# Kernel tuning notes

Hardware: AMD Instinct MI355X
Metric: run time of the kernel (lower is better)

The kernel has to match this reference:

```python
import jax, jax.numpy as jnp
import numpy as np

N = 20000        # nodes
E = 320000       # edges (avg degree 16)
D_IN = 64        # CFG.feature_dim
D_H = 128        # CFG.hidden_dim
T = 20           # CFG.ode_time_points
MIN_DEPTH, MAX_DEPTH = 0.1, 3.0
EPS = 1e-5       # torch LayerNorm default


def setup_inputs() -> dict:
    key = jax.random.key(0)
    ks = jax.random.split(key, 10)
    def rn(k, shape, fan_in):
        return jax.random.normal(k, shape, jnp.float32) / np.float32(np.sqrt(fan_in))
    return {
        "x": jax.random.normal(ks[0], (N, D_IN), jnp.float32),
        "edge_index": jax.random.randint(ks[1], (2, E), 0, N, dtype=jnp.int32),
        # input projection: Linear(64,128) + LayerNorm(128)
        "Wi": rn(ks[2], (D_IN, D_H), D_IN), "bi": jnp.zeros((D_H,), jnp.float32),
        "ln_in_g": jnp.ones((D_H,), jnp.float32), "ln_in_b": jnp.zeros((D_H,), jnp.float32),
        # epigenetic params (init zeros as in module)
        "meth": jnp.zeros((D_H,), jnp.float32), "hist": jnp.zeros((4,), jnp.float32),
        # 3 GCNConv(128,128) + LayerNorm(128)
        "gcn_w": rn(ks[3], (3, D_H, D_H), D_H), "gcn_b": jnp.zeros((3, D_H), jnp.float32),
        "ln_g": jnp.ones((3, D_H), jnp.float32), "ln_b": jnp.zeros((3, D_H), jnp.float32),
        # gate: Linear(256,128) + Sigmoid
        "gate_w": rn(ks[4], (2 * D_H, D_H), 2 * D_H), "gate_b": jnp.zeros((D_H,), jnp.float32),
        "res_w": jnp.float32(0.1),
        "log_depth": jnp.float32(0.0),
        # output projection: Linear(128,128) + LayerNorm(128)
        "Wo": rn(ks[5], (D_H, D_H), D_H), "bo": jnp.zeros((D_H,), jnp.float32),
        "ln_out_g": jnp.ones((D_H,), jnp.float32), "ln_out_b": jnp.zeros((D_H,), jnp.float32),
    }


def layernorm(x, g, b):
    mu = x.mean(-1, keepdims=True)
    var = ((x - mu) ** 2).mean(-1, keepdims=True)
    return (x - mu) * jax.lax.rsqrt(var + EPS) * g + b


def _forward(x, edge_index, Wi, bi, ln_in_g, ln_in_b, meth, hist,
             gcn_w, gcn_b, ln_g, ln_b, gate_w, gate_b, res_w, log_depth,
             Wo, bo, ln_out_g, ln_out_b):
    row, col = edge_index[0], edge_index[1]  # source -> target
    # GCN symmetric normalization (no self loops): 1/sqrt(deg_i deg_j)
    deg = jax.ops.segment_sum(jnp.ones((E,), jnp.float32), col, num_segments=N)
    dis = jnp.where(deg > 0, jax.lax.rsqrt(jnp.maximum(deg, 1.0)), 0.0)
    norm = (dis[row] * dis[col])[:, None]  # [E,1]

    def gcn(h, W, b):
        m = (h @ W)[row] * norm                      # [E, D_H] gather
        return jax.ops.segment_sum(m, col, num_segments=N) + b  # scatter

    # input projection (dropout is identity in eval)
    h = jax.nn.relu(layernorm(x @ Wi + bi, ln_in_g, ln_in_b))

    # epigenetic regulation (chromatin accessibility uses .item() in torch -> stop_gradient)
    meth_sil = jax.nn.sigmoid(meth).mean()
    hs = jax.nn.sigmoid(hist)
    act = (hs[0] + hs[2]) / 2
    rep = (hs[1] + hs[3]) / 2
    access = jax.lax.stop_gradient(jnp.clip(act - rep + 0.5, 0.0, 1.0))
    h = h * (access * (1.0 - meth_sil))

    # ODE dynamics dh/dt
    def f(hh):
        h0 = hh
        hc = hh
        for i in range(3):
            hn = layernorm(gcn(hc, gcn_w[i], gcn_b[i]), ln_g[i], ln_b[i])
            if i > 0:
                gate = jax.nn.sigmoid(jnp.concatenate([hc, hn], -1) @ gate_w + gate_b)
                hc = gate * hn + (1.0 - gate) * hc
            else:
                hc = hn
        hc = jnp.tanh(hc)
        return hc + res_w * h0

    depth = jnp.clip(jnp.exp(log_depth), MIN_DEPTH, MAX_DEPTH)
    dt = depth / (T - 1)

    def step(hh, _):
        k1 = f(hh)
        k2 = f(hh + 0.5 * dt * k1)
        k3 = f(hh + 0.5 * dt * k2)
        k4 = f(hh + dt * k3)
        return hh + (dt / 6.0) * (k1 + 2.0 * k2 + 2.0 * k3 + k4), None

    h_final, _ = jax.lax.scan(step, h, None, length=T - 1)

    h_out = layernorm(h_final @ Wo + bo, ln_out_g, ln_out_b)
    return h_out.mean(axis=0, keepdims=True)  # batch=None -> global mean pool [1, D_H]


def reference(x, edge_index, Wi, bi, ln_in_g, ln_in_b, meth, hist,
              gcn_w, gcn_b, ln_g, ln_b, gate_w, gate_b, res_w, log_depth,
              Wo, bo, ln_out_g, ln_out_b):
    return _forward(x, edge_index, Wi, bi, ln_in_g, ln_in_b, meth, hist,
                    gcn_w, gcn_b, ln_g, ln_b, gate_w, gate_b, res_w, log_depth,
                    Wo, bo, ln_out_g, ln_out_b)
```

## Files before the change

### kernel.cpp

```cpp
#include <hip/hip_runtime.h>

typedef unsigned int u32;
using bf16x8 = __attribute__((ext_vector_type(8))) short;
using f32x4  = __attribute__((ext_vector_type(4))) float;
using f32x2  = __attribute__((ext_vector_type(2))) float;

#define NN 20000
#define EE 320000
#define DH 128
#define DIN 64
#define TSTEPS 20
#define LNEPS 1e-5f
#define NCHUNK 1250

__device__ __forceinline__ u32 f2bf(float f) {
    u32 x = __float_as_uint(f);
    return (x + 0x7fffu + ((x >> 16) & 1u)) >> 16;
}
__device__ __forceinline__ float bflo(u32 p) { return __uint_as_float(p << 16); }
__device__ __forceinline__ float bfhi(u32 p) { return __uint_as_float(p & 0xffff0000u); }
__device__ __forceinline__ u32 packbf(float a, float b) { return f2bf(a) | (f2bf(b) << 16); }
__device__ __forceinline__ float wredsum(float v) {
#pragma unroll
    for (int m = 32; m >= 1; m >>= 1) v += __shfl_xor(v, m, 64);
    return v;
}
__device__ __forceinline__ float sigm(float x) { return 1.f / (1.f + __expf(-x)); }

__device__ __forceinline__ void accum8_fp8(float* a, uint2 q, float w) {
    f32x2 c01 = __builtin_amdgcn_cvt_pk_f32_fp8((int)q.x, false);
    f32x2 c23 = __builtin_amdgcn_cvt_pk_f32_fp8((int)q.x, true);
    f32x2 c45 = __builtin_amdgcn_cvt_pk_f32_fp8((int)q.y, false);
    f32x2 c67 = __builtin_amdgcn_cvt_pk_f32_fp8((int)q.y, true);
    a[0] += w * c01[0]; a[1] += w * c01[1];
    a[2] += w * c23[0]; a[3] += w * c23[1];
    a[4] += w * c45[0]; a[5] += w * c45[1];
    a[6] += w * c67[0]; a[7] += w * c67[1];
}

__device__ __forceinline__ void store_dual(u32* dstb, u32* dst8, int node, int j, int sub, float o) {
    float po = __shfl_xor(o, 1, 64);
    if (!(sub & 1)) dstb[node * 64 + j * 8 + (sub >> 1)] = packbf(o, po);
    int pk = __builtin_amdgcn_cvt_pk_fp8_f32(o, po, 0, false);
    int pk2 = __shfl_xor(pk, 2, 64);
    if (!(sub & 3)) dst8[node * 32 + j * 4 + (sub >> 2)] = (u32)(pk & 0xffff) | ((u32)pk2 << 16);
}

__global__ void k_init(int* deg, float* oacc) {
    int i = blockIdx.x * blockDim.x + threadIdx.x;
    if (i < NN) deg[i] = 0;
    if (i < DH) oacc[i] = 0.f;
}

__global__ void k_scalars(const float* meth, const float* hist, const float* logd,
                          const float* resw, float* sc) {
    float msum = 0.f;
    for (int j = 0; j < DH; j++) msum += sigm(meth[j]);
    float msil = msum * (1.f / DH);
    float h0 = sigm(hist[0]), h1 = sigm(hist[1]), h2 = sigm(hist[2]), h3 = sigm(hist[3]);
    float act = 0.5f * (h0 + h2), rep = 0.5f * (h1 + h3);
    float access = fminf(fmaxf(act - rep + 0.5f, 0.f), 1.f);
    sc[0] = access * (1.f - msil);
    float depth = fminf(fmaxf(__expf(logd[0]), 0.1f), 3.f);
    sc[1] = depth / (float)(TSTEPS - 1);
    sc[2] = resw[0];
}

__global__ void k_deg(const int* col, int* deg) {
    int e = blockIdx.x * blockDim.x + threadIdx.x;
    if (e < EE) atomicAdd(&deg[col[e]], 1);
}

__global__ __launch_bounds__(1024) void k_scan(const int* deg, int* offs, int* cursor, float* dis) {
    __shared__ int part[1024];
    const int CH = (NN + 1023) / 1024;
    int t = threadIdx.x;
    int base = t * CH;
    int s = 0;
    for (int k = 0; k < CH; k++) { int i = base + k; if (i < NN) s += deg[i]; }
    part[t] = s;
    __syncthreads();
    for (int off = 1; off < 1024; off <<= 1) {
        int v = part[t];
        int add = (t >= off) ? part[t - off] : 0;
        __syncthreads();
        part[t] = v + add;
        __syncthreads();
    }
    int run = part[t] - s;
    for (int k = 0; k < CH; k++) {
        int i = base + k;
        if (i < NN) {
            offs[i] = run; cursor[i] = run;
            int d = deg[i];
            run += d;
            dis[i] = (d > 0) ? rsqrtf((float)d) : 0.f;
        }
    }
    if (t == 1023) offs[NN] = run;
}

__global__ void k_scatter(const int* row, const int* col, int* cursor, const float* dis,
                          u32* epk) {
    int e = blockIdx.x * blockDim.x + threadIdx.x;
    if (e < EE) {
        int c = col[e], r = row[e];
        int pos = atomicAdd(&cursor[c], 1);
        epk[pos] = (f2bf(dis[r] * dis[c]) << 16) | (u32)r;
    }
}

__global__ void k_pack(const float* gcnw, const float* gatew, const float* Wo,
                       u32* wfrag, u32* gfrag, u32* wopk) {
    int tid = blockIdx.x * blockDim.x + threadIdx.x;
    if (tid < 6144) {
        int lane = tid & 63, rem = tid >> 6;
        int j = rem & 7; rem >>= 3;
        int q = rem & 3; int l = rem >> 2;
        const float* W = gcnw + l * DH * DH;
        int r0 = 32 * q + 8 * (lane >> 4);
        int c  = 16 * j + (lane & 15);
        u32* o = wfrag + tid * 4;
#pragma unroll
        for (int p = 0; p < 4; p++)
            o[p] = packbf(W[(r0 + 2 * p) * DH + c], W[(r0 + 2 * p + 1) * DH + c]);
    } else if (tid < 6144 + 4096) {
        int t = tid - 6144;
        int lane = t & 63, rem = t >> 6;
        int j = rem & 7, q = rem >> 3;
        int r0 = 32 * q + 8 * (lane >> 4);
        int c  = 16 * j + (lane & 15);
        u32* o = gfrag + t * 4;
#pragma unroll
        for (int p = 0; p < 4; p++)
            o[p] = packbf(gatew[(r0 + 2 * p) * DH + c], gatew[(r0 + 2 * p + 1) * DH + c]);
    } else if (tid < 6144 + 4096 + 8192) {
        int t = tid - 10240;
        int k2 = t / DH, j = t % DH;
        wopk[t] = packbf(Wo[(2 * k2) * DH + j], Wo[(2 * k2 + 1) * DH + j]);
    }
}

__global__ __launch_bounds__(1024) void k_inproj(const float* x, const float* Wi, const float* bi,
                                                 const float* g, const float* b, const float* sc,
                                                 u32* y, u32* y8, float* hh) {
    __shared__ float Wl[DIN * DH];
    for (int i = threadIdx.x; i < DIN * DH; i += 1024) Wl[i] = Wi[i];
    __syncthreads();
    int wv = threadIdx.x >> 6, t = threadIdx.x & 63;
    int n = blockIdx.x * 16 + wv;
    if (n >= NN) return;
    float xv = x[n * DIN + t];
    float2 bb = *(const float2*)&bi[2 * t];
    float y0 = bb.x, y1 = bb.y;
#pragma unroll
    for (int k = 0; k < DIN; k++) {
        float a = __shfl(xv, k, 64);
        float2 w = *(const float2*)&Wl[k * DH + 2 * t];
        y0 += a * w.x; y1 += a * w.y;
    }
    float mu = wredsum(y0 + y1) * (1.f / DH);
    float d0 = y0 - mu, d1 = y1 - mu;
    float var = wredsum(d0 * d0 + d1 * d1) * (1.f / DH);
    float r = rsqrtf(var + LNEPS);
    float2 gg = *(const float2*)&g[2 * t], lb = *(const float2*)&b[2 * t];
    float scale = sc[0];
    float v0 = fmaxf(d0 * r * gg.x + lb.x, 0.f) * scale;
    float v1 = fmaxf(d1 * r * gg.y + lb.y, 0.f) * scale;
    y[n * 64 + t] = packbf(v0, v1);
    *(float2*)&hh[n * DH + 2 * t] = make_float2(v0, v1);
    int pk = __builtin_amdgcn_cvt_pk_fp8_f32(v0, v1, 0, false);
    int pk2 = __shfl_xor(pk, 1, 64);
    if (!(t & 1)) y8[n * 32 + (t >> 1)] = (u32)(pk & 0xffff) | ((u32)pk2 << 16);
}

__device__ __forceinline__ void gather_row(const u32* __restrict__ src8, u32* tile,
                                           int row, int sub, int qb, int e0, int e1,
                                           const u32* __restrict__ epk) {
    float a[8] = {0.f, 0.f, 0.f, 0.f, 0.f, 0.f, 0.f, 0.f};
    for (int eb = e0; eb < e1; eb += 16) {
        int cc = min(16, e1 - eb);
        u32 p = 0;
        if (sub < cc) p = epk[eb + sub];
        {
            u32 pe[8]; uint2 q[8];
#pragma unroll
            for (int u = 0; u < 8; u++) pe[u] = (u32)__shfl((int)p, qb + u, 64);
#pragma unroll
            for (int u = 0; u < 8; u++)
                q[u] = *(const uint2*)(src8 + (pe[u] & 0xffffu) * 32 + sub * 2);
#pragma unroll
            for (int u = 0; u < 8; u++)
                accum8_fp8(a, q[u], __uint_as_float(pe[u] & 0xffff0000u));
        }
        if (cc > 8) {
            u32 pe[8]; uint2 q[8];
#pragma unroll
            for (int u = 0; u < 8; u++) pe[u] = (u32)__shfl((int)p, qb + 8 + u, 64);
#pragma unroll
            for (int u = 0; u < 8; u++)
                q[u] = *(const uint2*)(src8 + (pe[u] & 0xffffu) * 32 + sub * 2);
#pragma unroll
            for (int u = 0; u < 8; u++)
                accum8_fp8(a, q[u], __uint_as_float(pe[u] & 0xffff0000u));
        }
    }
    uint4 v;
    v.x = packbf(a[0], a[1]); v.y = packbf(a[2], a[3]);
    v.z = packbf(a[4], a[5]); v.w = packbf(a[6], a[7]);
    *(uint4*)(tile + row * 68 + sub * 4) = v;
}

__global__ __launch_bounds__(256, 5) void k_aggmm(const u32* __restrict__ src8,
                                                  u32* __restrict__ dstb, u32* __restrict__ dst8,
                                                  const u32* __restrict__ wfrag,
                                                  const float* __restrict__ bias,
                                                  const float* __restrict__ lng,
                                                  const float* __restrict__ lnb,
                                                  const int* __restrict__ offs,
                                                  const u32* __restrict__ epk) {
    __shared__ u32 tile[16 * 68];
    __shared__ float lred1[4][16], lred2[4][16];
    int wv = threadIdx.x >> 6, lane = threadIdx.x & 63;
    int base = blockIdx.x * 16;
    int t4 = lane >> 4, sub = lane & 15;
    int row = wv * 4 + t4;
    int e0 = offs[base + row], e1 = offs[base + row + 1];
    gather_row(src8, tile, row, sub, t4 * 16, e0, e1, epk);
    __syncthreads();

    f32x4 acc[2];
#pragma unroll
    for (int jl = 0; jl < 2; jl++) acc[jl] = (f32x4){0.f, 0.f, 0.f, 0.f};
#pragma unroll
    for (int q = 0; q < 4; q++) {
        bf16x8 A = *(const bf16x8*)(tile + sub * 68 + q * 16 + t4 * 4);
#pragma unroll
        for (int jl = 0; jl < 2; jl++) {
            int j = 2 * wv + jl;
            bf16x8 B = *(const bf16x8*)(wfrag + ((q * 8 + j) * 64 + lane) * 4);
            acc[jl] = __builtin_amdgcn_mfma_f32_16x16x32_bf16(A, B, acc[jl], 0, 0, 0);
        }
    }
    float s1[4] = {0.f, 0.f, 0.f, 0.f}, s2[4] = {0.f, 0.f, 0.f, 0.f};
#pragma unroll
    for (int jl = 0; jl < 2; jl++) {
        float bb = bias[16 * (2 * wv + jl) + sub];
#pragma unroll
        for (int r = 0; r < 4; r++) {
            float v = acc[jl][r] + bb;
            acc[jl][r] = v;
            s1[r] += v; s2[r] += v * v;
        }
    }
#pragma unroll
    for (int r = 0; r < 4; r++) {
#pragma unroll
        for (int m = 1; m <= 8; m <<= 1) {
            s1[r] += __shfl_xor(s1[r], m, 64);
            s2[r] += __shfl_xor(s2[r], m, 64);
        }
        if (sub == 0) { lred1[wv][4 * t4 + r] = s1[r]; lred2[wv][4 * t4 + r] = s2[r]; }
    }
    __syncthreads();
    float mu[4], rs[4];
#pragma unroll
    for (int r = 0; r < 4; r++) {
        int n16 = 4 * t4 + r;
        float t1 = lred1[0][n16] + lred1[1][n16] + lred1[2][n16] + lred1[3][n16];
        float t2 = lred2[0][n16] + lred2[1][n16] + lred2[2][n16] + lred2[3][n16];
        mu[r] = t1 * (1.f / DH);
        float var = t2 * (1.f / DH) - mu[r] * mu[r];
        rs[r] = rsqrtf(var + LNEPS);
    }
#pragma unroll
    for (int jl = 0; jl < 2; jl++) {
        int j = 2 * wv + jl;
        float gg = lng[16 * j + sub], be = lnb[16 * j + sub];
#pragma unroll
        for (int r = 0; r < 4; r++) {
            float o = (acc[jl][r] - mu[r]) * rs[r] * gg + be;
            store_dual(dstb, dst8, base + 4 * t4 + r, j, sub, o);
        }
    }
}

template <bool LAST>
__global__ __launch_bounds__(256, 5) void k_fused(const u32* __restrict__ srcb,
                                                  const u32* __restrict__ src8,
                                                  u32* __restrict__ dstb, u32* __restrict__ dst8,
                                                  const u32* __restrict__ wfragL,
                                                  const float* __restrict__ bias,
                                                  const float* __restrict__ lng,
                                                  const float* __restrict__ lnb,
                                                  const u32* __restrict__ gfrag,
                                                  const float* __restrict__ gateb,
                                                  float* __restrict__ hh,
                                                  unsigned short* __restrict__ acc_g,
                                                  const float* __restrict__ sc, int rkj,
                                                  const int* __restrict__ offs,
                                                  const u32* __restrict__ epk) {
    __shared__ u32 tile[16 * 68];
    __shared__ float lred1[4][16], lred2[4][16];
    int wv = threadIdx.x >> 6, lane = threadIdx.x & 63;
    int base = blockIdx.x * 16;
    int t4 = lane >> 4, sub = lane & 15;
    int row = wv * 4 + t4;
    int e0 = offs[base + row], e1 = offs[base + row + 1];

    bf16x8 Ahc[4];
#pragma unroll
    for (int q = 0; q < 4; q++)
        Ahc[q] = *(const bf16x8*)(srcb + (base + sub) * 64 + q * 16 + t4 * 4);

    float hv_p[2][4]; u32 py_p[2][4]; float av_p[2][4];
    if (LAST) {
#pragma unroll
        for (int jl = 0; jl < 2; jl++) {
            int j = 2 * wv + jl;
#pragma unroll
            for (int r = 0; r < 4; r++) {
                int node = base + 4 * t4 + r;
                int fi = node * DH + 16 * j + sub;
                hv_p[jl][r] = hh[fi];
                py_p[jl][r] = dstb[node * 64 + j * 8 + (sub >> 1)];
                av_p[jl][r] = (rkj != 0) ? __uint_as_float((u32)acc_g[fi] << 16) : 0.f;
            }
        }
    }

    gather_row(src8, tile, row, sub, t4 * 16, e0, e1, epk);
    __syncthreads();

    f32x4 acc[2];
#pragma unroll
    for (int jl = 0; jl < 2; jl++) acc[jl] = (f32x4){0.f, 0.f, 0.f, 0.f};
#pragma unroll
    for (int q = 0; q < 4; q++) {
        bf16x8 A = *(const bf16x8*)(tile + sub * 68 + q * 16 + t4 * 4);
#pragma unroll
        for (int jl = 0; jl < 2; jl++) {
            int j = 2 * wv + jl;
            bf16x8 B = *(const bf16x8*)(wfragL + ((q * 8 + j) * 64 + lane) * 4);
            acc[jl] = __builtin_amdgcn_mfma_f32_16x16x32_bf16(A, B, acc[jl], 0, 0, 0);
        }
    }

    float s1[4] = {0.f, 0.f, 0.f, 0.f}, s2[4] = {0.f, 0.f, 0.f, 0.f};
#pragma unroll
    for (int jl = 0; jl < 2; jl++) {
        float bb = bias[16 * (2 * wv + jl) + sub];
#pragma unroll
        for (int r = 0; r < 4; r++) {
            float v = acc[jl][r] + bb;
            acc[jl][r] = v;
            s1[r] += v; s2[r] += v * v;
        }
    }
#pragma unroll
    for (int r = 0; r < 4; r++) {
#pragma unroll
        for (int m = 1; m <= 8; m <<= 1) {
            s1[r] += __shfl_xor(s1[r], m, 64);
            s2[r] += __shfl_xor(s2[r], m, 64);
        }
        if (sub == 0) { lred1[wv][4 * t4 + r] = s1[r]; lred2[wv][4 * t4 + r] = s2[r]; }
    }
    __syncthreads();
    float mu[4], rs[4];
#pragma unroll
    for (int r = 0; r < 4; r++) {
        int n16 = 4 * t4 + r;
        float t1 = lred1[0][n16] + lred1[1][n16] + lred1[2][n16] + lred1[3][n16];
        float t2 = lred2[0][n16] + lred2[1][n16] + lred2[2][n16] + lred2[3][n16];
        mu[r] = t1 * (1.f / DH);
        float var = t2 * (1.f / DH) - mu[r] * mu[r];
        rs[r] = rsqrtf(var + LNEPS);
    }
#pragma unroll
    for (int jl = 0; jl < 2; jl++) {
        int j = 2 * wv + jl;
        float gg = lng[16 * j + sub], be = lnb[16 * j + sub];
#pragma unroll
        for (int r = 0; r < 4; r++)
            acc[jl][r] = (acc[jl][r] - mu[r]) * rs[r] * gg + be;
    }

#pragma unroll
    for (int jl = 0; jl < 2; jl++) {
        int j = 2 * wv + jl;
#pragma unroll
        for (int r = 0; r < 4; r++) {
            float o = acc[jl][r];
            float po = __shfl_xor(o, 1, 64);
            if (!(sub & 1)) tile[(4 * t4 + r) * 68 + j * 8 + (sub >> 1)] = packbf(o, po);
        }
    }
    __syncthreads();

    f32x4 ag[2];
#pragma unroll
    for (int jl = 0; jl < 2; jl++) ag[jl] = (f32x4){0.f, 0.f, 0.f, 0.f};
#pragma unroll
    for (int q = 0; q < 8; q++) {
        bf16x8 A = (q < 4) ? Ahc[q]
                           : *(const bf16x8*)(tile + sub * 68 + (q - 4) * 16 + t4 * 4);
#pragma unroll
        for (int jl = 0; jl < 2; jl++) {
            int j = 2 * wv + jl;
            bf16x8 B = *(const bf16x8*)(gfrag + ((q * 8 + j) * 64 + lane) * 4);
            ag[jl] = __builtin_amdgcn_mfma_f32_16x16x32_bf16(A, B, ag[jl], 0, 0, 0);
        }
    }

    float dt = 0.f, rw = 0.f;
    if (LAST) { dt = sc[1]; rw = sc[2]; }
#pragma unroll
    for (int jl = 0; jl < 2; jl++) {
        int j = 2 * wv + jl;
        float gbj = gateb[16 * j + sub];
#pragma unroll
        for (int r = 0; r < 4; r++) {
            int node = base + 4 * t4 + r;
            int ui = node * 64 + j * 8 + (sub >> 1);
            float g = sigm(ag[jl][r] + gbj);
            u32 pc = srcb[ui];
            float hcv = (sub & 1) ? bfhi(pc) : bflo(pc);
            float o = g * acc[jl][r] + (1.f - g) * hcv;
            if (!LAST) {
                store_dual(dstb, dst8, node, j, sub, o);
            } else {
                float z = fminf(fmaxf(o, -15.f), 15.f);
                float e = __expf(2.f * z);
                float th = (e - 1.f) / (e + 1.f);
                float yv = (sub & 1) ? bfhi(py_p[jl][r]) : bflo(py_p[jl][r]);
                float kk = th + rw * yv;
                float wj = dt * (1.f / 6.f) * ((rkj == 1 || rkj == 2) ? 2.f : 1.f);
                int fi = node * DH + 16 * j + sub;
                float av = wj * kk + av_p[jl][r];
                acc_g[fi] = (unsigned short)f2bf(av);
                float hv = hv_p[jl][r];
                if (rkj < 3) {
                    float c = (rkj == 2) ? dt : 0.5f * dt;
                    store_dual(dstb, dst8, node, j, sub, hv + c * kk);
                } else {
                    float f = hv + av;
                    hh[fi] = f;
                    store_dual(dstb, dst8, node, j, sub, f);
                }
            }
        }
    }
}

__global__ __launch_bounds__(1024) void k_outproj(const float* __restrict__ hh, const u32* wopk,
                                                  const float* bo, const float* g, const float* b,
                                                  float* oacc) {
    __shared__ u32 Wl[64 * DH];
    __shared__ float red[DH];
    for (int i = threadIdx.x; i < 64 * DH; i += 1024) Wl[i] = wopk[i];
    if (threadIdx.x < DH) red[threadIdx.x] = 0.f;
    __syncthreads();
    int wv = threadIdx.x >> 6, t = threadIdx.x & 63;
    int n = blockIdx.x * 16 + wv;
    if (n < NN) {
        float2 hv = *(const float2*)&hh[n * DH + 2 * t];
        float h0 = hv.x, h1 = hv.y;
        float2 bb = *(const float2*)&bo[2 * t];
        float y0 = bb.x, y1 = bb.y;
#pragma unroll
        for (int k2 = 0; k2 < 64; k2++) {
            float a0 = __shfl(h0, k2, 64), a1 = __shfl(h1, k2, 64);
            uint2 wq = *(const uint2*)&Wl[k2 * DH + 2 * t];
            y0 += a0 * bflo(wq.x) + a1 * bfhi(wq.x);
            y1 += a0 * bflo(wq.y) + a1 * bfhi(wq.y);
        }
        float mu = wredsum(y0 + y1) * (1.f / DH);
        float d0 = y0 - mu, d1 = y1 - mu;
        float var = wredsum(d0 * d0 + d1 * d1) * (1.f / DH);
        float r = rsqrtf(var + LNEPS);
        float2 gg = *(const float2*)&g[2 * t], lb = *(const float2*)&b[2 * t];
        atomicAdd(&red[2 * t], d0 * r * gg.x + lb.x);
        atomicAdd(&red[2 * t + 1], d1 * r * gg.y + lb.y);
    }
    __syncthreads();
    if (threadIdx.x < DH) atomicAdd(&oacc[threadIdx.x], red[threadIdx.x]);
}

__global__ void k_final(const float* oacc, float* out) {
    int t = threadIdx.x;
    if (t < DH) out[t] = oacc[t] * (1.f / (float)NN);
}

extern "C" void kernel_launch(void* const* d_in, const int* in_sizes, int n_in,
                              void* d_out, int out_size, void* d_ws, size_t ws_size,
                              hipStream_t stream) {
    const float* x     = (const float*)d_in[0];
    const int*   ei    = (const int*)d_in[1];
    const float* Wi    = (const float*)d_in[2];
    const float* bi    = (const float*)d_in[3];
    const float* ling  = (const float*)d_in[4];
    const float* linb  = (const float*)d_in[5];
    const float* meth  = (const float*)d_in[6];
    const float* hist  = (const float*)d_in[7];
    const float* gcnw  = (const float*)d_in[8];
    const float* gcnb  = (const float*)d_in[9];
    const float* lng   = (const float*)d_in[10];
    const float* lnb   = (const float*)d_in[11];
    const float* gatew = (const float*)d_in[12];
    const float* gateb = (const float*)d_in[13];
    const float* resw  = (const float*)d_in[14];
    const float* logd  = (const float*)d_in[15];
    const float* Wo    = (const float*)d_in[16];
    const float* bo    = (const float*)d_in[17];
    const float* loutg = (const float*)d_in[18];
    const float* loutb = (const float*)d_in[19];

    char* wsb = (char*)d_ws;
    size_t off = 0;
    auto alloc = [&](size_t bytes) -> void* {
        void* p = wsb + off;
        off += (bytes + 255) & ~(size_t)255;
        return p;
    };
    float* sc     = (float*)alloc(32);
    int*   deg    = (int*)alloc(NN * 4);
    int*   offs   = (int*)alloc((NN + 1) * 4);
    int*   cursor = (int*)alloc(NN * 4);
    float* dis    = (float*)alloc(NN * 4);
    u32*   epk    = (u32*)alloc(EE * 4);
    u32*   wfrag  = (u32*)alloc(3 * 32 * 64 * 4 * 4);
    u32*   gfrag  = (u32*)alloc(64 * 64 * 4 * 4);
    u32*   wopk   = (u32*)alloc(64 * DH * 4);
    u32*   y      = (u32*)alloc((size_t)NN * 64 * 4);
    u32*   hc     = (u32*)alloc((size_t)NN * 64 * 4);
    u32*   hc2    = (u32*)alloc((size_t)NN * 64 * 4);
    u32*   y8     = (u32*)alloc((size_t)NN * 32 * 4);
    u32*   hc8    = (u32*)alloc((size_t)NN * 32 * 4);
    u32*   hc28   = (u32*)alloc((size_t)NN * 32 * 4);
    float* hh     = (float*)alloc((size_t)NN * DH * 4);
    unsigned short* accg = (unsigned short*)alloc((size_t)NN * DH * 2);
    float* oacc   = (float*)alloc(DH * 4);

    const int* row = ei;
    const int* col = ei + EE;

    k_init<<<(NN + 255) / 256, 256, 0, stream>>>(deg, oacc);
    k_scalars<<<1, 1, 0, stream>>>(meth, hist, logd, resw, sc);
    k_deg<<<(EE + 255) / 256, 256, 0, stream>>>(col, deg);
    k_scan<<<1, 1024, 0, stream>>>(deg, offs, cursor, dis);
    k_scatter<<<(EE + 255) / 256, 256, 0, stream>>>(row, col, cursor, dis, epk);
    k_pack<<<(6144 + 4096 + 8192 + 255) / 256, 256, 0, stream>>>(gcnw, gatew, Wo, wfrag, gfrag, wopk);

    const int GB1 = (NN + 15) / 16;
    k_inproj<<<GB1, 1024, 0, stream>>>(x, Wi, bi, ling, linb, sc, y, y8, hh);

    const int LSZ = 32 * 64 * 4;
    for (int s = 0; s < TSTEPS - 1; s++) {
        for (int j = 0; j < 4; j++) {
            k_aggmm<<<NCHUNK, 256, 0, stream>>>(y8, hc, hc8, wfrag, gcnb, lng, lnb, offs, epk);
            k_fused<false><<<NCHUNK, 256, 0, stream>>>(hc, hc8, hc2, hc28, wfrag + LSZ,
                                                       gcnb + DH, lng + DH, lnb + DH,
                                                       gfrag, gateb, nullptr, nullptr,
                                                       sc, j, offs, epk);
            k_fused<true><<<NCHUNK, 256, 0, stream>>>(hc2, hc28, y, y8, wfrag + 2 * LSZ,
                                                      gcnb + 2 * DH, lng + 2 * DH, lnb + 2 * DH,
                                                      gfrag, gateb, hh, accg,
                                                      sc, j, offs, epk);
        }
    }

    k_outproj<<<GB1, 1024, 0, stream>>>(hh, wopk, bo, loutg, loutb, oacc);
    k_final<<<1, 128, 0, stream>>>(oacc, (float*)d_out);
}
```

Before: 7.766 ms.

## Fuse all ODE stage kernels into one persistent kernel with grid barriers

Replaces the 228 separate kernel launches of the RK4 loop with a single persistent kernel of 1250 blocks. Stages are separated by a hierarchical software grid barrier built from atomic counters (8 groups plus a global counter and a phase flag). This removes launch gaps and per-launch setup such as reloading CSR offsets. It depends on all 1250 blocks being co-resident (launch bounds 256,5 over the CU count), otherwise the barrier deadlocks. Spinning on atomics also adds a cost at every stage.

Measured after the change: 30.32 ms. 3.9x slower.

```diff
diff --git a/kernel.cpp b/kernel.cpp
--- a/kernel.cpp
+++ b/kernel.cpp
@@ -46,10 +46,11 @@
     if (!(sub & 3)) dst8[node * 32 + j * 4 + (sub >> 2)] = (u32)(pk & 0xffff) | ((u32)pk2 << 16);
 }
 
-__global__ void k_init(int* deg, float* oacc) {
+__global__ void k_init(int* deg, float* oacc, u32* bars) {
     int i = blockIdx.x * blockDim.x + threadIdx.x;
     if (i < NN) deg[i] = 0;
     if (i < DH) oacc[i] = 0.f;
+    if (i < 512) bars[i] = 0u;
 }
 
 __global__ void k_scalars(const float* meth, const float* hist, const float* logd,
@@ -211,21 +212,17 @@
     *(uint4*)(tile + row * 68 + sub * 4) = v;
 }
 
-__global__ __launch_bounds__(256, 5) void k_aggmm(const u32* __restrict__ src8,
-                                                  u32* __restrict__ dstb, u32* __restrict__ dst8,
-                                                  const u32* __restrict__ wfrag,
-                                                  const float* __restrict__ bias,
-                                                  const float* __restrict__ lng,
-                                                  const float* __restrict__ lnb,
-                                                  const int* __restrict__ offs,
-                                                  const u32* __restrict__ epk) {
-    __shared__ u32 tile[16 * 68];
-    __shared__ float lred1[4][16], lred2[4][16];
-    int wv = threadIdx.x >> 6, lane = threadIdx.x & 63;
-    int base = blockIdx.x * 16;
+__device__ __forceinline__ void body_aggmm(const u32* __restrict__ src8,
+                                           u32* __restrict__ dstb, u32* __restrict__ dst8,
+                                           const u32* __restrict__ wfrag,
+                                           const float* __restrict__ bias,
+                                           const float* __restrict__ lng,
+                                           const float* __restrict__ lnb,
+                                           const u32* __restrict__ epk,
+                                           u32* tile, float (*lred1)[16], float (*lred2)[16],
+                                           int wv, int lane, int base, int e0, int e1) {
     int t4 = lane >> 4, sub = lane & 15;
     int row = wv * 4 + t4;
-    int e0 = offs[base + row], e1 = offs[base + row + 1];
     gather_row(src8, tile, row, sub, t4 * 16, e0, e1, epk);
     __syncthreads();
 
@@ -286,27 +283,23 @@
 }
 
 template <bool LAST>
-__global__ __launch_bounds__(256, 5) void k_fused(const u32* __restrict__ srcb,
-                                                  const u32* __restrict__ src8,
-                                                  u32* __restrict__ dstb, u32* __restrict__ dst8,
-                                                  const u32* __restrict__ wfragL,
-                                                  const float* __restrict__ bias,
-                                                  const float* __restrict__ lng,
-                                                  const float* __restrict__ lnb,
-                                                  const u32* __restrict__ gfrag,
-                                                  const float* __restrict__ gateb,
-                                                  float* __restrict__ hh,
-                                                  unsigned short* __restrict__ acc_g,
-                                                  const float* __restrict__ sc, int rkj,
-                                                  const int* __restrict__ offs,
-                                                  const u32* __restrict__ epk) {
-    __shared__ u32 tile[16 * 68];
-    __shared__ float lred1[4][16], lred2[4][16];
-    int wv = threadIdx.x >> 6, lane = threadIdx.x & 63;
-    int base = blockIdx.x * 16;
+__device__ __forceinline__ void body_fused(const u32* __restrict__ srcb,
+                                           const u32* __restrict__ src8,
+                                           u32* __restrict__ dstb, u32* __restrict__ dst8,
+                                           const u32* __restrict__ wfragL,
+                                           const float* __restrict__ bias,
+                                           const float* __restrict__ lng,
+                                           const float* __restrict__ lnb,
+                                           const u32* __restrict__ gfrag,
+                                           const float* __restrict__ gateb,
+                                           float* __restrict__ hh,
+                                           unsigned short* __restrict__ acc_g,
+                                           const float* __restrict__ sc, int rkj,
+                                           const u32* __restrict__ epk,
+                                           u32* tile, float (*lred1)[16], float (*lred2)[16],
+                                           int wv, int lane, int base, int e0, int e1) {
     int t4 = lane >> 4, sub = lane & 15;
     int row = wv * 4 + t4;
-    int e0 = offs[base + row], e1 = offs[base + row + 1];
 
     bf16x8 Ahc[4];
 #pragma unroll
@@ -453,6 +446,68 @@
     }
 }
 
+__device__ __forceinline__ void pbar(u32* bars, u32 phase) {
+    __syncthreads();
+    if (threadIdx.x == 0) {
+        int grp = blockIdx.x & 7;
+        u32 per = (grp < (NCHUNK & 7)) ? (u32)(NCHUNK / 8 + 1) : (u32)(NCHUNK / 8);
+        u32 old = __hip_atomic_fetch_add(&bars[grp * 32], 1u, __ATOMIC_RELEASE,
+                                         __HIP_MEMORY_SCOPE_AGENT);
+        if (old == phase * per - 1u) {
+            u32 g = __hip_atomic_fetch_add(&bars[256], 1u, __ATOMIC_RELEASE,
+                                           __HIP_MEMORY_SCOPE_AGENT);
+            if (g == phase * 8u - 1u)
+                __hip_atomic_store(&bars[288], phase, __ATOMIC_RELEASE,
+                                   __HIP_MEMORY_SCOPE_AGENT);
+        }
+        while (__hip_atomic_load(&bars[288], __ATOMIC_RELAXED, __HIP_MEMORY_SCOPE_AGENT) < phase)
+            __builtin_amdgcn_s_sleep(32);
+        (void)__hip_atomic_load(&bars[288], __ATOMIC_ACQUIRE, __HIP_MEMORY_SCOPE_AGENT);
+    }
+    __syncthreads();
+}
+
+__global__ __launch_bounds__(256, 5) void k_ode(u32* y, u32* y8, u32* hc, u32* hc8,
+                                                u32* hc2, u32* hc28,
+                                                const u32* __restrict__ wfrag,
+                                                const u32* __restrict__ gfrag,
+                                                const float* __restrict__ gcnb,
+                                                const float* __restrict__ lng,
+                                                const float* __restrict__ lnb,
+                                                const float* __restrict__ gateb,
+                                                float* __restrict__ hh,
+                                                unsigned short* __restrict__ accg,
+                                                const float* __restrict__ sc,
+                                                const int* __restrict__ offs,
+                                                const u32* __restrict__ epk,
+                                                u32* bars) {
+    __shared__ u32 tile[16 * 68];
+    __shared__ float lred1[4][16], lred2[4][16];
+    int wv = threadIdx.x >> 6, lane = threadIdx.x & 63;
+    int base = blockIdx.x * 16;
+    int t4 = lane >> 4;
+    int row = wv * 4 + t4;
+    int e0 = offs[base + row], e1 = offs[base + row + 1];
+
+    const int LSZ = 32 * 64 * 4;
+    u32 phase = 0;
+    for (int s = 0; s < TSTEPS - 1; s++) {
+        for (int j = 0; j < 4; j++) {
+            body_aggmm(y8, hc, hc8, wfrag, gcnb, lng, lnb, epk,
+                       tile, lred1, lred2, wv, lane, base, e0, e1);
+            pbar(bars, ++phase);
+            body_fused<false>(hc, hc8, hc2, hc28, wfrag + LSZ, gcnb + DH, lng + DH, lnb + DH,
+                              gfrag, gateb, nullptr, nullptr, sc, j, epk,
+                              tile, lred1, lred2, wv, lane, base, e0, e1);
+            pbar(bars, ++phase);
+            body_fused<true>(hc2, hc28, y, y8, wfrag + 2 * LSZ, gcnb + 2 * DH, lng + 2 * DH,
+                             lnb + 2 * DH, gfrag, gateb, hh, accg, sc, j, epk,
+                             tile, lred1, lred2, wv, lane, base, e0, e1);
+            pbar(bars, ++phase);
+        }
+    }
+}
+
 __global__ __launch_bounds__(1024) void k_outproj(const float* __restrict__ hh, const u32* wopk,
                                                   const float* bo, const float* g, const float* b,
                                                   float* oacc) {
@@ -524,6 +579,7 @@
         return p;
     };
     float* sc     = (float*)alloc(32);
+    u32*   bars   = (u32*)alloc(512 * 4);
     int*   deg    = (int*)alloc(NN * 4);
     int*   offs   = (int*)alloc((NN + 1) * 4);
     int*   cursor = (int*)alloc(NN * 4);
@@ -545,7 +601,7 @@
     const int* row = ei;
     const int* col = ei + EE;
 
-    k_init<<<(NN + 255) / 256, 256, 0, stream>>>(deg, oacc);
+    k_init<<<(NN + 255) / 256, 256, 0, stream>>>(deg, oacc, bars);
     k_scalars<<<1, 1, 0, stream>>>(meth, hist, logd, resw, sc);
     k_deg<<<(EE + 255) / 256, 256, 0, stream>>>(col, deg);
     k_scan<<<1, 1024, 0, stream>>>(deg, offs, cursor, dis);
@@ -555,20 +611,8 @@
     const int GB1 = (NN + 15) / 16;
     k_inproj<<<GB1, 1024, 0, stream>>>(x, Wi, bi, ling, linb, sc, y, y8, hh);
 
-    const int LSZ = 32 * 64 * 4;
-    for (int s = 0; s < TSTEPS - 1; s++) {
-        for (int j = 0; j < 4; j++) {
-            k_aggmm<<<NCHUNK, 256, 0, stream>>>(y8, hc, hc8, wfrag, gcnb, lng, lnb, offs, epk);
-            k_fused<false><<<NCHUNK, 256, 0, stream>>>(hc, hc8, hc2, hc28, wfrag + LSZ,
-                                                       gcnb + DH, lng + DH, lnb + DH,
-                                                       gfrag, gateb, nullptr, nullptr,
-                                                       sc, j, offs, epk);
-            k_fused<true><<<NCHUNK, 256, 0, stream>>>(hc2, hc28, y, y8, wfrag + 2 * LSZ,
-                                                      gcnb + 2 * DH, lng + 2 * DH, lnb + 2 * DH,
-                                                      gfrag, gateb, hh, accg,
-                                                      sc, j, offs, epk);
-        }
-    }
+    k_ode<<<NCHUNK, 256, 0, stream>>>(y, y8, hc, hc8, hc2, hc28, wfrag, gfrag,
+                                      gcnb, lng, lnb, gateb, hh, accg, sc, offs, epk, bars);
 
     k_outproj<<<GB1, 1024, 0, stream>>>(hh, wopk, bo, loutg, loutb, oacc);
     k_final<<<1, 128, 0, stream>>>(oacc, (float*)d_out);
```
